# Optimization experiments

Measured on AMD Instinct MI355X. Metric: run time of the kernel, lower is better.

The kernel has to match this reference:

```python
import jax, jax.numpy as jnp
import numpy as np

N_NODES = 100000

def gcn_conv(x, W, b, src, dst, deg_isqrt):
    # x: [N, Fin] -> lin -> [N, Fout]; aggregate src->dst with sym norm; + bias
    h = x @ W                                   # [N, Fout]
    norm = deg_isqrt[src] * deg_isqrt[dst]      # [E+N]
    msg = h[src] * norm[:, None]                # [E+N, Fout]
    out = jax.ops.segment_sum(msg, dst, num_segments=N_NODES)
    return out + b

def setup_inputs() -> dict:
    key = jax.random.key(0)
    k1, k2, k3, k4 = jax.random.split(key, 4)
    x = jax.random.normal(k1, (N_NODES, 256), dtype=jnp.float32)
    edge_index = jax.random.randint(k2, (2, 3200000), 0, N_NODES, dtype=jnp.int32)
    # Glorot-ish params for GCNConv(256->16) and GCNConv(16->1)
    W1 = jax.random.normal(k3, (256, 16), dtype=jnp.float32) * (1.0 / np.sqrt(256))
    b1 = jnp.zeros((16,), dtype=jnp.float32)
    W2 = jax.random.normal(k4, (16, 1), dtype=jnp.float32) * (1.0 / np.sqrt(16))
    b2 = jnp.zeros((1,), dtype=jnp.float32)
    return {"x": x, "edge_index": edge_index, "W1": W1, "b1": b1, "W2": W2, "b2": b2}

def reference(x, edge_index, W1, b1, W2, b2):
    # GCNConv adds self-loops then symmetric normalization deg^{-1/2}
    loops = jnp.arange(N_NODES, dtype=edge_index.dtype)
    src = jnp.concatenate([edge_index[0], loops])
    dst = jnp.concatenate([edge_index[1], loops])
    deg = jax.ops.segment_sum(jnp.ones_like(src, dtype=x.dtype), dst, num_segments=N_NODES)
    deg_isqrt = jnp.where(deg > 0, jax.lax.rsqrt(deg), 0.0)

    h = gcn_conv(x, W1, b1, src, dst, deg_isqrt)
    h = jax.nn.relu(h)
    # dropout(p=0.5, train=self.training): eval mode -> identity (deterministic reference)
    out = gcn_conv(h, W2, b2, src, dst, deg_isqrt)
    return out  # [N, 1]
```

## Files before the change

kernel.cpp:

```cpp
#include <hip/hip_runtime.h>
#include <hip/hip_fp16.h>


#define SBSH 8
#define SBCAP 10240
#define HPAD 400
#define BINTHREADS 1024
#define ITEMS 32

__global__ void k_init(int* __restrict__ gcur, int Bsb) {
    int i = blockIdx.x * blockDim.x + threadIdx.x;
    if (i < Bsb) gcur[i] = i * SBCAP;
}

__global__ __launch_bounds__(BINTHREADS) void k_p1(
    const int* __restrict__ src, const int* __restrict__ dst,
    int* __restrict__ gcur, int* __restrict__ pairs, int E, int Bsb)
{
    __shared__ int hist[HPAD];
    const int t = threadIdx.x;
    const int base4 = blockIdx.x * (BINTHREADS * ITEMS / 4);
    for (int i = t; i < HPAD; i += BINTHREADS) hist[i] = 0;
    __syncthreads();

    int4 dd[ITEMS / 4];
    #pragma unroll
    for (int r = 0; r < ITEMS / 4; ++r) {
        const int i4 = base4 + r * BINTHREADS + t;
        const int i = i4 << 2;
        int4 v;
        if (i + 3 < E) v = ((const int4*)dst)[i4];
        else {
            v.x = (i     < E) ? dst[i]     : -1;
            v.y = (i + 1 < E) ? dst[i + 1] : -1;
            v.z = (i + 2 < E) ? dst[i + 2] : -1;
            v.w = (i + 3 < E) ? dst[i + 3] : -1;
        }
        dd[r] = v;
        if (v.x >= 0) atomicAdd(&hist[v.x >> SBSH], 1);
        if (v.y >= 0) atomicAdd(&hist[v.y >> SBSH], 1);
        if (v.z >= 0) atomicAdd(&hist[v.z >> SBSH], 1);
        if (v.w >= 0) atomicAdd(&hist[v.w >> SBSH], 1);
    }
    __syncthreads();
    for (int i = t; i < Bsb; i += BINTHREADS) {
        int c = hist[i];
        hist[i] = c ? atomicAdd(&gcur[i], c) : 0;
    }
    __syncthreads();
    #pragma unroll
    for (int r = 0; r < ITEMS / 4; ++r) {
        const int i4 = base4 + r * BINTHREADS + t;
        const int i = i4 << 2;
        int4 s;
        if (i + 3 < E) s = ((const int4*)src)[i4];
        else {
            s.x = (i     < E) ? src[i]     : 0;
            s.y = (i + 1 < E) ? src[i + 1] : 0;
            s.z = (i + 2 < E) ? src[i + 2] : 0;
            s.w = (i + 3 < E) ? src[i + 3] : 0;
        }
        int4 v = dd[r];
        if (v.x >= 0) { int p = atomicAdd(&hist[v.x >> SBSH], 1); pairs[p] = (s.x << SBSH) | (v.x & 255); }
        if (v.y >= 0) { int p = atomicAdd(&hist[v.y >> SBSH], 1); pairs[p] = (s.y << SBSH) | (v.y & 255); }
        if (v.z >= 0) { int p = atomicAdd(&hist[v.z >> SBSH], 1); pairs[p] = (s.z << SBSH) | (v.z & 255); }
        if (v.w >= 0) { int p = atomicAdd(&hist[v.w >> SBSH], 1); pairs[p] = (s.w << SBSH) | (v.w & 255); }
    }
}

__global__ __launch_bounds__(1024) void k_sortsb(
    int* __restrict__ pairs, const int* __restrict__ gcur,
    int* __restrict__ rowp, float* __restrict__ isq, int N)
{
    __shared__ int e[SBCAP];
    __shared__ int hist[256];
    __shared__ int cur[256];
    __shared__ int wsum[4];
    const int t = threadIdx.x, sb = blockIdx.x;
    const int beg = sb * SBCAP;
    const int cnt = gcur[sb] - beg;
    if (t < 256) hist[t] = 0;
    __syncthreads();
    for (int i = t; i < cnt; i += 1024) {
        int p = pairs[beg + i];
        e[i] = p;
        atomicAdd(&hist[p & 255], 1);
    }
    __syncthreads();
    int c = 0, v = 0;
    if (t < 256) {
        const int lane = t & 63, w = t >> 6;
        c = hist[t];
        v = c;
        #pragma unroll
        for (int off = 1; off < 64; off <<= 1) {
            int u = __shfl_up(v, off, 64);
            if (lane >= off) v += u;
        }
        if (lane == 63) wsum[w] = v;
    }
    __syncthreads();
    if (t < 256) {
        const int w = t >> 6;
        int add = 0;
        #pragma unroll
        for (int i = 0; i < 3; ++i) if (i < w) add += wsum[i];
        int inc = v + add;
        int exc = inc - c;
        cur[t] = exc;
        rowp[sb * 257 + t] = exc;
        if (t == 255) rowp[sb * 257 + 256] = inc;
        int n = (sb << SBSH) + t;
        if (n < N) isq[n] = rsqrtf((float)(c + 1));
    }
    __syncthreads();
    for (int i = t; i < cnt; i += 1024) {
        int p = e[i];
        int pos = atomicAdd(&cur[p & 255], 1);
        pairs[beg + pos] = p >> SBSH;
    }
}

__global__ __launch_bounds__(256) void k_lin1(
    const float* __restrict__ x, const float* __restrict__ W1,
    const float* __restrict__ isq, __half* __restrict__ hs16, int N)
{
    __shared__ float wL[256 * 16];
    {
        const float4* w4 = (const float4*)W1;
        float4* s4 = (float4*)wL;
        for (int i = threadIdx.x; i < 1024; i += 256) s4[i] = w4[i];
    }
    __syncthreads();
    const int gid = blockIdx.x * 256 + threadIdx.x;
    const int n = gid >> 2, q = gid & 3;
    if (n >= N) return;
    const float4* xr = (const float4*)(x + ((size_t)n << 8));
    const float4* wb = (const float4*)wL + q;
    float a0 = 0.f, a1 = 0.f, a2 = 0.f, a3 = 0.f;
    #pragma unroll 8
    for (int k4 = 0; k4 < 64; ++k4) {
        float4 xa = xr[k4];
        float4 w0 = wb[(k4 * 4 + 0) * 4];
        float4 w1 = wb[(k4 * 4 + 1) * 4];
        float4 w2 = wb[(k4 * 4 + 2) * 4];
        float4 w3 = wb[(k4 * 4 + 3) * 4];
        a0 += xa.x * w0.x + xa.y * w1.x + xa.z * w2.x + xa.w * w3.x;
        a1 += xa.x * w0.y + xa.y * w1.y + xa.z * w2.y + xa.w * w3.y;
        a2 += xa.x * w0.z + xa.y * w1.z + xa.z * w2.z + xa.w * w3.z;
        a3 += xa.x * w0.w + xa.y * w1.w + xa.z * w2.w + xa.w * w3.w;
    }
    const float iq = isq[n];
    __half2 h0 = __floats2half2_rn(a0 * iq, a1 * iq);
    __half2 h1 = __floats2half2_rn(a2 * iq, a3 * iq);
    __half2* o = (__half2*)&hs16[n * 16 + q * 4];
    o[0] = h0;
    o[1] = h1;
}

__global__ __launch_bounds__(256) void k_agg1(
    const int* __restrict__ sorted, const int* __restrict__ rowp,
    const __half* __restrict__ hs16, const float* __restrict__ isq,
    const float* __restrict__ b1, const float* __restrict__ W2,
    float* __restrict__ ts, int N)
{
    const int t = threadIdx.x, g = blockIdx.x;
    const int l = t >> 2, q = t & 3;
    const int n = g * 64 + l;
    if (n >= N) return;
    const int sb = n >> SBSH, L = n & 255;
    const int rbeg = sb * SBCAP + rowp[sb * 257 + L];
    const int rend = sb * SBCAP + rowp[sb * 257 + L + 1];
    const float2* h2 = (const float2*)hs16;
    float a0 = 0.f, a1 = 0.f, a2 = 0.f, a3 = 0.f;
    int j = rbeg;
    for (; j + 2 <= rend; j += 2) {
        int s0 = sorted[j], s1 = sorted[j + 1];
        float2 ra = h2[s0 * 4 + q];
        float2 rb = h2[s1 * 4 + q];
        union { float f; __half2 h; } ca0, ca1, cb0, cb1;
        ca0.f = ra.x; ca1.f = ra.y; cb0.f = rb.x; cb1.f = rb.y;
        float2 fa0 = __half22float2(ca0.h), fa1 = __half22float2(ca1.h);
        float2 fb0 = __half22float2(cb0.h), fb1 = __half22float2(cb1.h);
        a0 += fa0.x + fb0.x; a1 += fa0.y + fb0.y;
        a2 += fa1.x + fb1.x; a3 += fa1.y + fb1.y;
    }
    if (j < rend) {
        int s0 = sorted[j];
        float2 ra = h2[s0 * 4 + q];
        union { float f; __half2 h; } ca0, ca1;
        ca0.f = ra.x; ca1.f = ra.y;
        float2 fa0 = __half22float2(ca0.h), fa1 = __half22float2(ca1.h);
        a0 += fa0.x; a1 += fa0.y; a2 += fa1.x; a3 += fa1.y;
    }
    {
        float2 rs = h2[(size_t)n * 4 + q];
        union { float f; __half2 h; } c0, c1;
        c0.f = rs.x; c1.f = rs.y;
        float2 f0 = __half22float2(c0.h), f1 = __half22float2(c1.h);
        a0 += f0.x; a1 += f0.y; a2 += f1.x; a3 += f1.y;
    }
    const float iq = isq[n];
    const int f0i = q * 4;
    float p = fmaxf(a0 * iq + b1[f0i + 0], 0.f) * W2[f0i + 0]
            + fmaxf(a1 * iq + b1[f0i + 1], 0.f) * W2[f0i + 1]
            + fmaxf(a2 * iq + b1[f0i + 2], 0.f) * W2[f0i + 2]
            + fmaxf(a3 * iq + b1[f0i + 3], 0.f) * W2[f0i + 3];
    p += __shfl_xor(p, 1, 4);
    p += __shfl_xor(p, 2, 4);
    if (q == 0) ts[n] = p * iq;
}

__global__ __launch_bounds__(256) void k_agg2(
    const int* __restrict__ sorted, const int* __restrict__ rowp,
    const float* __restrict__ ts, const float* __restrict__ isq,
    const float* __restrict__ b2, float* __restrict__ out, int N)
{
    const int n = blockIdx.x * 256 + threadIdx.x;
    if (n >= N) return;
    const int sb = n >> SBSH, L = n & 255;
    const int rbeg = sb * SBCAP + rowp[sb * 257 + L];
    const int rend = sb * SBCAP + rowp[sb * 257 + L + 1];
    float acc = ts[n];
    int j = rbeg;
    for (; j + 4 <= rend; j += 4) {
        int s0 = sorted[j], s1 = sorted[j + 1], s2 = sorted[j + 2], s3 = sorted[j + 3];
        acc += (ts[s0] + ts[s1]) + (ts[s2] + ts[s3]);
    }
    for (; j < rend; ++j) acc += ts[sorted[j]];
    out[n] = acc * isq[n] + b2[0];
}

extern "C" void kernel_launch(void* const* d_in, const int* in_sizes, int n_in,
                              void* d_out, int out_size, void* d_ws, size_t ws_size,
                              hipStream_t stream) {
    const float* x  = (const float*)d_in[0];
    const int*   ei = (const int*)d_in[1];
    const float* W1 = (const float*)d_in[2];
    const float* b1 = (const float*)d_in[3];
    const float* W2 = (const float*)d_in[4];
    const float* b2 = (const float*)d_in[5];
    const int N = in_sizes[0] / 256;
    const int E = in_sizes[1] / 2;
    const int* src = ei;
    const int* dst = ei + E;
    const int Bsb = (N + 255) >> SBSH;

    char* w = (char*)d_ws;
    float*  isq   = (float*)w;  w += (size_t)N * 4;
    int*    gcur  = (int*)w;    w += HPAD * 4;
    int*    pairs = (int*)w;    w += (size_t)Bsb * SBCAP * 4;
    int*    rowp  = (int*)w;    w += (size_t)Bsb * 257 * 4;
    __half* hs16  = (__half*)w; w += (size_t)N * 32;
    float*  ts    = (float*)w;  w += (size_t)N * 4;
    float*  out   = (float*)d_out;

    k_init<<<(Bsb + 255) / 256, 256, 0, stream>>>(gcur, Bsb);

    const int nbBin = (E + BINTHREADS * ITEMS - 1) / (BINTHREADS * ITEMS);
    k_p1<<<nbBin, BINTHREADS, 0, stream>>>(src, dst, gcur, pairs, E, Bsb);

    k_sortsb<<<Bsb, 1024, 0, stream>>>(pairs, gcur, rowp, isq, N);

    k_lin1<<<(N * 4 + 255) / 256, 256, 0, stream>>>(x, W1, isq, hs16, N);

    k_agg1<<<(N + 63) / 64, 256, 0, stream>>>(pairs, rowp, hs16, isq, b1, W2, ts, N);
    k_agg2<<<(N + 255) / 256, 256, 0, stream>>>(pairs, rowp, ts, isq, b2, out, N);
}
```

Before: 315.4 us.

## Fuse superbucket sort and both aggregations into one cooperative kernel

The per-superbucket sort, first-layer aggregation and second-layer aggregation become a single cooperative kernel with a grid barrier between the layers. Sorted sources and row pointers stay in shared memory instead of being written back and re-read from global memory. Degrees are now counted with global atomics during binning, so lin1 can compute the inverse square roots without waiting for the sort. The costs are one global atomic per edge, a grid-wide sync, and the requirement that all 391 blocks of 512 threads with about 43KB of shared memory each are resident together.

```diff
diff --git a/kernel.cpp b/kernel.cpp
--- a/kernel.cpp
+++ b/kernel.cpp
@@ -1,5 +1,8 @@
 #include <hip/hip_runtime.h>
 #include <hip/hip_fp16.h>
+#include <hip/hip_cooperative_groups.h>
+
+namespace cg = cooperative_groups;
 
 
 #define SBSH 8
@@ -7,6 +10,8 @@
 #define HPAD 400
 #define BINTHREADS 1024
 #define ITEMS 32
+#define CTH 512
+#define STAGE (SBCAP / CTH)
 
 __global__ void k_init(int* __restrict__ gcur, int Bsb) {
     int i = blockIdx.x * blockDim.x + threadIdx.x;
@@ -15,7 +20,8 @@
 
 __global__ __launch_bounds__(BINTHREADS) void k_p1(
     const int* __restrict__ src, const int* __restrict__ dst,
-    int* __restrict__ gcur, int* __restrict__ pairs, int E, int Bsb)
+    int* __restrict__ gcur, int* __restrict__ pairs, int* __restrict__ deg,
+    int E, int Bsb)
 {
     __shared__ int hist[HPAD];
     const int t = threadIdx.x;
@@ -37,10 +43,10 @@
             v.w = (i + 3 < E) ? dst[i + 3] : -1;
         }
         dd[r] = v;
-        if (v.x >= 0) atomicAdd(&hist[v.x >> SBSH], 1);
-        if (v.y >= 0) atomicAdd(&hist[v.y >> SBSH], 1);
-        if (v.z >= 0) atomicAdd(&hist[v.z >> SBSH], 1);
-        if (v.w >= 0) atomicAdd(&hist[v.w >> SBSH], 1);
+        if (v.x >= 0) { atomicAdd(&hist[v.x >> SBSH], 1); atomicAdd(&deg[v.x], 1); }
+        if (v.y >= 0) { atomicAdd(&hist[v.y >> SBSH], 1); atomicAdd(&deg[v.y], 1); }
+        if (v.z >= 0) { atomicAdd(&hist[v.z >> SBSH], 1); atomicAdd(&deg[v.z], 1); }
+        if (v.w >= 0) { atomicAdd(&hist[v.w >> SBSH], 1); atomicAdd(&deg[v.w], 1); }
     }
     __syncthreads();
     for (int i = t; i < Bsb; i += BINTHREADS) {
@@ -68,62 +74,10 @@
     }
 }
 
-__global__ __launch_bounds__(1024) void k_sortsb(
-    int* __restrict__ pairs, const int* __restrict__ gcur,
-    int* __restrict__ rowp, float* __restrict__ isq, int N)
-{
-    __shared__ int e[SBCAP];
-    __shared__ int hist[256];
-    __shared__ int cur[256];
-    __shared__ int wsum[4];
-    const int t = threadIdx.x, sb = blockIdx.x;
-    const int beg = sb * SBCAP;
-    const int cnt = gcur[sb] - beg;
-    if (t < 256) hist[t] = 0;
-    __syncthreads();
-    for (int i = t; i < cnt; i += 1024) {
-        int p = pairs[beg + i];
-        e[i] = p;
-        atomicAdd(&hist[p & 255], 1);
-    }
-    __syncthreads();
-    int c = 0, v = 0;
-    if (t < 256) {
-        const int lane = t & 63, w = t >> 6;
-        c = hist[t];
-        v = c;
-        #pragma unroll
-        for (int off = 1; off < 64; off <<= 1) {
-            int u = __shfl_up(v, off, 64);
-            if (lane >= off) v += u;
-        }
-        if (lane == 63) wsum[w] = v;
-    }
-    __syncthreads();
-    if (t < 256) {
-        const int w = t >> 6;
-        int add = 0;
-        #pragma unroll
-        for (int i = 0; i < 3; ++i) if (i < w) add += wsum[i];
-        int inc = v + add;
-        int exc = inc - c;
-        cur[t] = exc;
-        rowp[sb * 257 + t] = exc;
-        if (t == 255) rowp[sb * 257 + 256] = inc;
-        int n = (sb << SBSH) + t;
-        if (n < N) isq[n] = rsqrtf((float)(c + 1));
-    }
-    __syncthreads();
-    for (int i = t; i < cnt; i += 1024) {
-        int p = e[i];
-        int pos = atomicAdd(&cur[p & 255], 1);
-        pairs[beg + pos] = p >> SBSH;
-    }
-}
-
 __global__ __launch_bounds__(256) void k_lin1(
     const float* __restrict__ x, const float* __restrict__ W1,
-    const float* __restrict__ isq, __half* __restrict__ hs16, int N)
+    const int* __restrict__ deg, float* __restrict__ isq,
+    __half* __restrict__ hs16, int N)
 {
     __shared__ float wL[256 * 16];
     {
@@ -150,7 +104,8 @@
         a2 += xa.x * w0.z + xa.y * w1.z + xa.z * w2.z + xa.w * w3.z;
         a3 += xa.x * w0.w + xa.y * w1.w + xa.z * w2.w + xa.w * w3.w;
     }
-    const float iq = isq[n];
+    const float iq = rsqrtf((float)(deg[n] + 1));
+    if (q == 0) isq[n] = iq;
     __half2 h0 = __floats2half2_rn(a0 * iq, a1 * iq);
     __half2 h1 = __floats2half2_rn(a2 * iq, a3 * iq);
     __half2* o = (__half2*)&hs16[n * 16 + q * 4];
@@ -158,77 +113,131 @@
     o[1] = h1;
 }
 
-__global__ __launch_bounds__(256) void k_agg1(
-    const int* __restrict__ sorted, const int* __restrict__ rowp,
+__global__ __launch_bounds__(CTH, 4) void k_coop(
+    const int* __restrict__ pairs, const int* __restrict__ gcur,
     const __half* __restrict__ hs16, const float* __restrict__ isq,
     const float* __restrict__ b1, const float* __restrict__ W2,
-    float* __restrict__ ts, int N)
+    const float* __restrict__ b2, float* __restrict__ ts,
+    float* __restrict__ out, int N)
 {
-    const int t = threadIdx.x, g = blockIdx.x;
-    const int l = t >> 2, q = t & 3;
-    const int n = g * 64 + l;
-    if (n >= N) return;
-    const int sb = n >> SBSH, L = n & 255;
-    const int rbeg = sb * SBCAP + rowp[sb * 257 + L];
-    const int rend = sb * SBCAP + rowp[sb * 257 + L + 1];
+    cg::grid_group grid = cg::this_grid();
+    __shared__ int e[SBCAP];
+    __shared__ int hist[256];
+    __shared__ int rstart[257];
+    __shared__ int cur[256];
+    __shared__ int wsum[4];
+    const int t = threadIdx.x, sb = blockIdx.x;
+    const int beg = sb * SBCAP;
+    const int cnt = gcur[sb] - beg;
+
+    if (t < 256) hist[t] = 0;
+    __syncthreads();
+    int rg[STAGE];
+    #pragma unroll
+    for (int j = 0; j < STAGE; ++j) {
+        int i = t + j * CTH;
+        int p = (i < cnt) ? pairs[beg + i] : -1;
+        rg[j] = p;
+        if (p >= 0) atomicAdd(&hist[p & 255], 1);
+    }
+    __syncthreads();
+    int c = 0, v = 0;
+    if (t < 256) {
+        const int lane = t & 63, w = t >> 6;
+        c = hist[t];
+        v = c;
+        #pragma unroll
+        for (int off = 1; off < 64; off <<= 1) {
+            int u = __shfl_up(v, off, 64);
+            if (lane >= off) v += u;
+        }
+        if (lane == 63) wsum[w] = v;
+    }
+    __syncthreads();
+    if (t < 256) {
+        const int w = t >> 6;
+        int add = 0;
+        #pragma unroll
+        for (int i = 0; i < 3; ++i) if (i < w) add += wsum[i];
+        int inc = v + add, exc = inc - c;
+        cur[t] = exc;
+        rstart[t] = exc;
+        if (t == 255) rstart[256] = inc;
+    }
+    __syncthreads();
+    #pragma unroll
+    for (int j = 0; j < STAGE; ++j) {
+        int p = rg[j];
+        if (p >= 0) {
+            int pos = atomicAdd(&cur[p & 255], 1);
+            e[pos] = p >> SBSH;
+        }
+    }
+    __syncthreads();
+
+    const int q = t & 3;
+    const int f0i = q * 4;
+    const float b10 = b1[f0i], b11 = b1[f0i + 1], b12 = b1[f0i + 2], b13 = b1[f0i + 3];
+    const float w20 = W2[f0i], w21 = W2[f0i + 1], w22 = W2[f0i + 2], w23 = W2[f0i + 3];
     const float2* h2 = (const float2*)hs16;
-    float a0 = 0.f, a1 = 0.f, a2 = 0.f, a3 = 0.f;
-    int j = rbeg;
-    for (; j + 2 <= rend; j += 2) {
-        int s0 = sorted[j], s1 = sorted[j + 1];
-        float2 ra = h2[s0 * 4 + q];
-        float2 rb = h2[s1 * 4 + q];
-        union { float f; __half2 h; } ca0, ca1, cb0, cb1;
-        ca0.f = ra.x; ca1.f = ra.y; cb0.f = rb.x; cb1.f = rb.y;
-        float2 fa0 = __half22float2(ca0.h), fa1 = __half22float2(ca1.h);
-        float2 fb0 = __half22float2(cb0.h), fb1 = __half22float2(cb1.h);
-        a0 += fa0.x + fb0.x; a1 += fa0.y + fb0.y;
-        a2 += fa1.x + fb1.x; a3 += fa1.y + fb1.y;
-    }
-    if (j < rend) {
-        int s0 = sorted[j];
-        float2 ra = h2[s0 * 4 + q];
-        union { float f; __half2 h; } ca0, ca1;
-        ca0.f = ra.x; ca1.f = ra.y;
-        float2 fa0 = __half22float2(ca0.h), fa1 = __half22float2(ca1.h);
-        a0 += fa0.x; a1 += fa0.y; a2 += fa1.x; a3 += fa1.y;
-    }
-    {
-        float2 rs = h2[(size_t)n * 4 + q];
-        union { float f; __half2 h; } c0, c1;
-        c0.f = rs.x; c1.f = rs.y;
-        float2 f0 = __half22float2(c0.h), f1 = __half22float2(c1.h);
-        a0 += f0.x; a1 += f0.y; a2 += f1.x; a3 += f1.y;
-    }
-    const float iq = isq[n];
-    const int f0i = q * 4;
-    float p = fmaxf(a0 * iq + b1[f0i + 0], 0.f) * W2[f0i + 0]
-            + fmaxf(a1 * iq + b1[f0i + 1], 0.f) * W2[f0i + 1]
-            + fmaxf(a2 * iq + b1[f0i + 2], 0.f) * W2[f0i + 2]
-            + fmaxf(a3 * iq + b1[f0i + 3], 0.f) * W2[f0i + 3];
-    p += __shfl_xor(p, 1, 4);
-    p += __shfl_xor(p, 2, 4);
-    if (q == 0) ts[n] = p * iq;
-}
-
-__global__ __launch_bounds__(256) void k_agg2(
-    const int* __restrict__ sorted, const int* __restrict__ rowp,
-    const float* __restrict__ ts, const float* __restrict__ isq,
-    const float* __restrict__ b2, float* __restrict__ out, int N)
-{
-    const int n = blockIdx.x * 256 + threadIdx.x;
-    if (n >= N) return;
-    const int sb = n >> SBSH, L = n & 255;
-    const int rbeg = sb * SBCAP + rowp[sb * 257 + L];
-    const int rend = sb * SBCAP + rowp[sb * 257 + L + 1];
-    float acc = ts[n];
-    int j = rbeg;
-    for (; j + 4 <= rend; j += 4) {
-        int s0 = sorted[j], s1 = sorted[j + 1], s2 = sorted[j + 2], s3 = sorted[j + 3];
-        acc += (ts[s0] + ts[s1]) + (ts[s2] + ts[s3]);
-    }
-    for (; j < rend; ++j) acc += ts[sorted[j]];
-    out[n] = acc * isq[n] + b2[0];
+    #pragma unroll
+    for (int half = 0; half < 2; ++half) {
+        const int l = (t >> 2) + half * 128;
+        const int n = (sb << SBSH) + l;
+        if (n < N) {
+            float a0 = 0.f, a1 = 0.f, a2 = 0.f, a3 = 0.f;
+            const int rb = rstart[l], re = rstart[l + 1];
+            int j = rb;
+            for (; j + 2 <= re; j += 2) {
+                int s0 = e[j], s1 = e[j + 1];
+                float2 ra = h2[s0 * 4 + q];
+                float2 rb2 = h2[s1 * 4 + q];
+                union { float f; __half2 h; } ca0, ca1, cb0, cb1;
+                ca0.f = ra.x; ca1.f = ra.y; cb0.f = rb2.x; cb1.f = rb2.y;
+                float2 fa0 = __half22float2(ca0.h), fa1 = __half22float2(ca1.h);
+                float2 fb0 = __half22float2(cb0.h), fb1 = __half22float2(cb1.h);
+                a0 += fa0.x + fb0.x; a1 += fa0.y + fb0.y;
+                a2 += fa1.x + fb1.x; a3 += fa1.y + fb1.y;
+            }
+            if (j < re) {
+                int s0 = e[j];
+                float2 ra = h2[s0 * 4 + q];
+                union { float f; __half2 h; } ca0, ca1;
+                ca0.f = ra.x; ca1.f = ra.y;
+                float2 fa0 = __half22float2(ca0.h), fa1 = __half22float2(ca1.h);
+                a0 += fa0.x; a1 += fa0.y; a2 += fa1.x; a3 += fa1.y;
+            }
+            {
+                float2 rs = h2[(size_t)n * 4 + q];
+                union { float f; __half2 h; } c0, c1;
+                c0.f = rs.x; c1.f = rs.y;
+                float2 f0 = __half22float2(c0.h), f1 = __half22float2(c1.h);
+                a0 += f0.x; a1 += f0.y; a2 += f1.x; a3 += f1.y;
+            }
+            const float iq = isq[n];
+            float p = fmaxf(a0 * iq + b10, 0.f) * w20
+                    + fmaxf(a1 * iq + b11, 0.f) * w21
+                    + fmaxf(a2 * iq + b12, 0.f) * w22
+                    + fmaxf(a3 * iq + b13, 0.f) * w23;
+            p += __shfl_xor(p, 1, 4);
+            p += __shfl_xor(p, 2, 4);
+            if (q == 0) ts[n] = p * iq;
+        }
+    }
+
+    __threadfence();
+    grid.sync();
+
+    const int rr = t & 1;
+    const int l2 = t >> 1;
+    const int n2 = (sb << SBSH) + l2;
+    float acc = 0.f;
+    if (n2 < N) {
+        const int rb = rstart[l2], re = rstart[l2 + 1];
+        for (int j = rb + rr; j < re; j += 2) acc += ts[e[j]];
+    }
+    acc += __shfl_xor(acc, 1, 2);
+    if (n2 < N && rr == 0) out[n2] = (acc + ts[n2]) * isq[n2] + b2[0];
 }
 
 extern "C" void kernel_launch(void* const* d_in, const int* in_sizes, int n_in,
@@ -247,23 +256,24 @@
     const int Bsb = (N + 255) >> SBSH;
 
     char* w = (char*)d_ws;
+    int*    deg   = (int*)w;    w += (size_t)N * 4;
     float*  isq   = (float*)w;  w += (size_t)N * 4;
     int*    gcur  = (int*)w;    w += HPAD * 4;
     int*    pairs = (int*)w;    w += (size_t)Bsb * SBCAP * 4;
-    int*    rowp  = (int*)w;    w += (size_t)Bsb * 257 * 4;
     __half* hs16  = (__half*)w; w += (size_t)N * 32;
     float*  ts    = (float*)w;  w += (size_t)N * 4;
     float*  out   = (float*)d_out;
 
+    hipMemsetAsync(deg, 0, (size_t)N * 4, stream);
     k_init<<<(Bsb + 255) / 256, 256, 0, stream>>>(gcur, Bsb);
 
     const int nbBin = (E + BINTHREADS * ITEMS - 1) / (BINTHREADS * ITEMS);
-    k_p1<<<nbBin, BINTHREADS, 0, stream>>>(src, dst, gcur, pairs, E, Bsb);
-
-    k_sortsb<<<Bsb, 1024, 0, stream>>>(pairs, gcur, rowp, isq, N);
-
-    k_lin1<<<(N * 4 + 255) / 256, 256, 0, stream>>>(x, W1, isq, hs16, N);
-
-    k_agg1<<<(N + 63) / 64, 256, 0, stream>>>(pairs, rowp, hs16, isq, b1, W2, ts, N);
-    k_agg2<<<(N + 255) / 256, 256, 0, stream>>>(pairs, rowp, ts, isq, b2, out, N);
-}
+    k_p1<<<nbBin, BINTHREADS, 0, stream>>>(src, dst, gcur, pairs, deg, E, Bsb);
+
+    k_lin1<<<(N * 4 + 255) / 256, 256, 0, stream>>>(x, W1, deg, isq, hs16, N);
+
+    void* args[] = {(void*)&pairs, (void*)&gcur, (void*)&hs16, (void*)&isq,
+                    (void*)&b1, (void*)&W2, (void*)&b2, (void*)&ts,
+                    (void*)&out, (void*)&N};
+    hipLaunchCooperativeKernel((void*)k_coop, dim3(Bsb), dim3(CTH), args, 0, stream);
+}
```

Result: slower. 526.9 us (+67.1%).
